# Performance work log

Hardware: AMD Instinct MI355X
Metric: run time of the kernel (lower is better)

The kernel has to match this reference:

```python
import jax, jax.numpy as jnp
import numpy as np

TEMPERATURE = 0.07
NEG_INF = -9e15
EPS = 1e-8  # matches torch F.cosine_similarity eps default


def setup_inputs() -> dict:
    key = jax.random.key(0)
    k1, k2 = jax.random.split(key)
    N, D = 4096, 512
    z1 = jax.random.normal(k1, (N, D), dtype=jnp.float32)
    z2 = jax.random.normal(k2, (N, D), dtype=jnp.float32)
    return {"z1": z1, "z2": z2}


def reference(z1, z2):
    N = z1.shape[0]
    z = jnp.concatenate([z1, z2], axis=0)  # [2N, D]
    # cosine similarity as normalized GEMM (torch clamps norm by eps)
    norm = jnp.maximum(jnp.linalg.norm(z, axis=-1, keepdims=True), EPS)
    zn = z / norm
    sim = (zn @ zn.T) / TEMPERATURE  # [2N, 2N]
    two_n = 2 * N
    idx = jnp.arange(two_n)
    sim = sim.at[idx, idx].set(NEG_INF)
    # positives: diag(sim, N) then diag(sim, -N)
    pos_upper = sim[idx[:N], idx[:N] + N]
    pos_lower = sim[idx[:N] + N, idx[:N]]
    positives = jnp.concatenate([pos_upper, pos_lower], axis=0)  # [2N]
    loss = -positives + jax.scipy.special.logsumexp(sim, axis=1)
    return loss.mean()
```

## Files before the change

kernel.cpp:

```cpp
#include <hip/hip_runtime.h>
#include <hip/hip_bf16.h>

#define N_ROWS 4096
#define TWO_N 8192
#define DIM 512
#define BK 32
#define NKS (DIM / BK)
#define INV_T 14.285714285714286f
#define LOG2E 1.4426950408889634f
#define C_LOG2E 20.60992915555662f
#define INV_SQRT_T 3.7796447300922722f

typedef __bf16 bf16x8 __attribute__((ext_vector_type(8)));
typedef float f32x4 __attribute__((ext_vector_type(4)));

#define ASYNC_COPY16(gp, lp)                                                     \
  __builtin_amdgcn_global_load_lds((const __attribute__((address_space(1))) void*)(gp), \
                                   (__attribute__((address_space(3))) void*)(lp), 16, 0, 0)

#define VMCNT(n) asm volatile("s_waitcnt vmcnt(" #n ")" ::: "memory")

__global__ __launch_bounds__(256) void k_prep(const float* __restrict__ z1,
                                              const float* __restrict__ z2,
                                              __hip_bfloat16* __restrict__ zn,
                                              float* __restrict__ posbuf,
                                              float* __restrict__ rowsum) {
  const int t = threadIdx.x;
  const int wv = t >> 6, lane = t & 63;
  const int r = blockIdx.x * 4 + wv;
  if (blockIdx.x < 32) rowsum[blockIdx.x * 256 + t] = 0.f;

  const float4* p1 = reinterpret_cast<const float4*>(z1 + (size_t)r * DIM) + (lane << 1);
  const float4* p2 = reinterpret_cast<const float4*>(z2 + (size_t)r * DIM) + (lane << 1);
  float4 a0 = p1[0], a1 = p1[1];
  float4 b0 = p2[0], b1 = p2[1];

  float s1 = a0.x * a0.x + a0.y * a0.y + a0.z * a0.z + a0.w * a0.w
           + a1.x * a1.x + a1.y * a1.y + a1.z * a1.z + a1.w * a1.w;
  float s2 = b0.x * b0.x + b0.y * b0.y + b0.z * b0.z + b0.w * b0.w
           + b1.x * b1.x + b1.y * b1.y + b1.z * b1.z + b1.w * b1.w;
  float sd = a0.x * b0.x + a0.y * b0.y + a0.z * b0.z + a0.w * b0.w
           + a1.x * b1.x + a1.y * b1.y + a1.z * b1.z + a1.w * b1.w;
#pragma unroll
  for (int off = 1; off < 64; off <<= 1) {
    s1 += __shfl_xor(s1, off, 64);
    s2 += __shfl_xor(s2, off, 64);
    sd += __shfl_xor(sd, off, 64);
  }
  const float sc1 = INV_SQRT_T / fmaxf(sqrtf(s1), 1e-8f);
  const float sc2 = INV_SQRT_T / fmaxf(sqrtf(s2), 1e-8f);

  bf16x8 o;
  o[0] = (__bf16)(a0.x * sc1); o[1] = (__bf16)(a0.y * sc1);
  o[2] = (__bf16)(a0.z * sc1); o[3] = (__bf16)(a0.w * sc1);
  o[4] = (__bf16)(a1.x * sc1); o[5] = (__bf16)(a1.y * sc1);
  o[6] = (__bf16)(a1.z * sc1); o[7] = (__bf16)(a1.w * sc1);
  *reinterpret_cast<bf16x8*>(zn + (size_t)r * DIM + (lane << 3)) = o;

  o[0] = (__bf16)(b0.x * sc2); o[1] = (__bf16)(b0.y * sc2);
  o[2] = (__bf16)(b0.z * sc2); o[3] = (__bf16)(b0.w * sc2);
  o[4] = (__bf16)(b1.x * sc2); o[5] = (__bf16)(b1.y * sc2);
  o[6] = (__bf16)(b1.z * sc2); o[7] = (__bf16)(b1.w * sc2);
  *reinterpret_cast<bf16x8*>(zn + (size_t)(r + N_ROWS) * DIM + (lane << 3)) = o;

  if (lane == 0) posbuf[r] = sd * sc1 * sc2;
}

__global__ __launch_bounds__(256, 3) void k_lse(const __hip_bfloat16* __restrict__ Zn,
                                                float* __restrict__ rowsum) {
  __shared__ char smem[49152] __attribute__((aligned(16)));
  const int tid  = threadIdx.x;
  const int wave = tid >> 6;
  const int lane = tid & 63;
  const int cl   = lane & 15;
  const int q    = lane >> 4;

  const int b = (blockIdx.x & 7) * 260 + (blockIdx.x >> 3);

  int rt = (int)((129.0f - sqrtf(16641.0f - 8.0f * (float)b)) * 0.5f);
  if (rt > 63) rt = 63;
  if (rt < 0) rt = 0;
  while (rt > 0 && 64 * rt - rt * (rt - 1) / 2 > b) rt--;
  while (64 * (rt + 1) - (rt + 1) * rt / 2 <= b) rt++;
  const int ct = rt + (b - (64 * rt - rt * (rt - 1) / 2));

  const int wr = (wave >> 1) * 64;
  const int wc = (wave & 1) * 64;

  const int g0 = tid, g1 = tid + 256;
  const int r0 = g0 >> 2, k0 = (((g0 & 3) - ((g0 >> 4) & 3)) & 3) * 8;
  const int r1 = g1 >> 2, k1 = (((g1 & 3) - ((g1 >> 4) & 3)) & 3) * 8;
  const size_t aoff0 = (size_t)(rt * 128 + r0) * DIM + k0;
  const size_t aoff1 = (size_t)(rt * 128 + r1) * DIM + k1;
  const size_t boff0 = (size_t)(ct * 128 + r0) * DIM + k0;
  const size_t boff1 = (size_t)(ct * 128 + r1) * DIM + k1;

  f32x4 acc[4][4] = {};
  const int kx = ((q + (cl >> 2)) & 3) * 8;

#define STAGE(bufi, ko)                                                    \
  {                                                                        \
    char* dA = smem + (bufi) * 16384 + wave * 1024;                        \
    char* dB = smem + (bufi) * 16384 + 8192 + wave * 1024;                 \
    ASYNC_COPY16(Zn + aoff0 + (ko), dA);                                   \
    ASYNC_COPY16(Zn + aoff1 + (ko), dA + 4096);                            \
    ASYNC_COPY16(Zn + boff0 + (ko), dB);                                   \
    ASYNC_COPY16(Zn + boff1 + (ko), dB + 4096);                            \
  }

  STAGE(0, 0);
  STAGE(1, BK);
  int cur = 0;
  for (int ks = 0; ks < NKS; ks++) {
    if (ks + 1 < NKS) { VMCNT(4); } else { VMCNT(0); }
    __builtin_amdgcn_s_barrier();
    asm volatile("" ::: "memory");
    if (ks + 2 < NKS) {
      int nb = cur + 2; if (nb >= 3) nb -= 3;
      STAGE(nb, (ks + 2) * BK);
    }

    const char* sA = smem + cur * 16384;
    const char* sB = sA + 8192;
    bf16x8 af[4], bfr[4];
#pragma unroll
    for (int i = 0; i < 4; i++)
      af[i] = *reinterpret_cast<const bf16x8*>(sA + ((wr + i * 16 + cl) * BK + kx) * 2);
#pragma unroll
    for (int j = 0; j < 4; j++)
      bfr[j] = *reinterpret_cast<const bf16x8*>(sB + ((wc + j * 16 + cl) * BK + kx) * 2);
#pragma unroll
    for (int i = 0; i < 4; i++)
#pragma unroll
      for (int j = 0; j < 4; j++)
        acc[i][j] = __builtin_amdgcn_mfma_f32_16x16x32_bf16(af[i], bfr[j], acc[i][j], 0, 0, 0);

    cur = (cur + 1 == 3) ? 0 : cur + 1;
  }
#undef STAGE

  const bool diagw = (rt == ct) && (wr == wc);
  float psum[4][4];
#pragma unroll
  for (int i = 0; i < 4; i++)
#pragma unroll
    for (int r = 0; r < 4; r++) psum[i][r] = 0.f;
  float colp[4] = {0.f, 0.f, 0.f, 0.f};

#pragma unroll
  for (int i = 0; i < 4; i++)
#pragma unroll
    for (int j = 0; j < 4; j++)
#pragma unroll
      for (int r = 0; r < 4; r++) {
        float e = exp2f(fmaf(acc[i][j][r], LOG2E, -C_LOG2E));
        if (diagw && (i == j) && (cl == q * 4 + r)) e = 0.f;
        psum[i][r] += e;
        colp[j] += e;
      }

#pragma unroll
  for (int i = 0; i < 4; i++)
#pragma unroll
    for (int r = 0; r < 4; r++) {
      float v = psum[i][r];
      v += __shfl_xor(v, 1, 64);
      v += __shfl_xor(v, 2, 64);
      v += __shfl_xor(v, 4, 64);
      v += __shfl_xor(v, 8, 64);
      if (cl == 0) atomicAdd(&rowsum[rt * 128 + wr + i * 16 + q * 4 + r], v);
    }

  if (rt != ct) {
#pragma unroll
    for (int j = 0; j < 4; j++) {
      float v = colp[j];
      v += __shfl_xor(v, 16, 64);
      v += __shfl_xor(v, 32, 64);
      if (q == 0) atomicAdd(&rowsum[ct * 128 + wc + j * 16 + cl], v);
    }
  }
}

__global__ void k_final(const float* __restrict__ rowsum, const float* __restrict__ posbuf,
                        float* __restrict__ out) {
  __shared__ float red[16];
  const int t = threadIdx.x;
  float s = 0.f;
#pragma unroll
  for (int it = 0; it < TWO_N / 1024; it++) {
    const int row = it * 1024 + t;
    float v = logf(rowsum[row]);
    if (row < N_ROWS) v -= 2.f * posbuf[row];
    s += v;
  }
#pragma unroll
  for (int off = 32; off > 0; off >>= 1) s += __shfl_down(s, off, 64);
  if ((t & 63) == 0) red[t >> 6] = s;
  __syncthreads();
  if (t == 0) {
    float tot = 0.f;
#pragma unroll
    for (int i = 0; i < 16; i++) tot += red[i];
    out[0] = tot / (float)TWO_N + INV_T;
  }
}

extern "C" void kernel_launch(void* const* d_in, const int* in_sizes, int n_in,
                              void* d_out, int out_size, void* d_ws, size_t ws_size,
                              hipStream_t stream) {
  const float* z1 = (const float*)d_in[0];
  const float* z2 = (const float*)d_in[1];
  float* out = (float*)d_out;
  char* ws = (char*)d_ws;

  __hip_bfloat16* zn = (__hip_bfloat16*)ws;
  float* rowsum = (float*)(ws + 8388608);
  float* posbuf = (float*)(ws + 8421376);

  k_prep<<<1024, 256, 0, stream>>>(z1, z2, zn, posbuf, rowsum);
  k_lse<<<2080, 256, 0, stream>>>(zn, rowsum);
  k_final<<<1, 1024, 0, stream>>>(rowsum, posbuf, out);
}
```

Baseline: 130.3 us.

## Use 256x256 tiles with 8 waves and phased double-buffered LDS pipeline

Moves the symmetric-GEMM LSE kernel from 128x128 tiles with 4 waves to 256x256 tiles with 8 waves, 128 KB of double-buffered LDS, and a BK=64 XOR-swizzled layout. The main loop becomes barrier-separated phases that issue the next stage's async loads alongside the MFMA work, and raise wave priority during the MFMA bursts. The larger tiles are meant to cut global and LDS traffic per flop and the atomic count. In exchange there are only 528 blocks, so fewer tiles to balance across CUs, wasted work on the diagonal tiles, and higher LDS and register use.

```diff
diff --git a/kernel.cpp b/kernel.cpp
--- a/kernel.cpp
+++ b/kernel.cpp
@@ -4,8 +4,6 @@
 #define N_ROWS 4096
 #define TWO_N 8192
 #define DIM 512
-#define BK 32
-#define NKS (DIM / BK)
 #define INV_T 14.285714285714286f
 #define LOG2E 1.4426950408889634f
 #define C_LOG2E 20.60992915555662f
@@ -66,101 +64,122 @@
   if (lane == 0) posbuf[r] = sd * sc1 * sc2;
 }
 
-__global__ __launch_bounds__(256, 3) void k_lse(const __hip_bfloat16* __restrict__ Zn,
+__global__ __launch_bounds__(512, 2) void k_lse(const __hip_bfloat16* __restrict__ Zn,
                                                 float* __restrict__ rowsum) {
-  __shared__ char smem[49152] __attribute__((aligned(16)));
+  __shared__ char smem[131072] __attribute__((aligned(16)));
   const int tid  = threadIdx.x;
   const int wave = tid >> 6;
   const int lane = tid & 63;
   const int cl   = lane & 15;
   const int q    = lane >> 4;
-
-  const int b = (blockIdx.x & 7) * 260 + (blockIdx.x >> 3);
-
-  int rt = (int)((129.0f - sqrtf(16641.0f - 8.0f * (float)b)) * 0.5f);
-  if (rt > 63) rt = 63;
+  const int wm   = wave >> 2;
+  const int wn   = wave & 3;
+
+  const int b = (blockIdx.x & 7) * 66 + (blockIdx.x >> 3);
+  int rt = (int)((65.0f - sqrtf(4225.0f - 8.0f * (float)b)) * 0.5f);
   if (rt < 0) rt = 0;
-  while (rt > 0 && 64 * rt - rt * (rt - 1) / 2 > b) rt--;
-  while (64 * (rt + 1) - (rt + 1) * rt / 2 <= b) rt++;
-  const int ct = rt + (b - (64 * rt - rt * (rt - 1) / 2));
-
-  const int wr = (wave >> 1) * 64;
-  const int wc = (wave & 1) * 64;
-
-  const int g0 = tid, g1 = tid + 256;
-  const int r0 = g0 >> 2, k0 = (((g0 & 3) - ((g0 >> 4) & 3)) & 3) * 8;
-  const int r1 = g1 >> 2, k1 = (((g1 & 3) - ((g1 >> 4) & 3)) & 3) * 8;
-  const size_t aoff0 = (size_t)(rt * 128 + r0) * DIM + k0;
-  const size_t aoff1 = (size_t)(rt * 128 + r1) * DIM + k1;
-  const size_t boff0 = (size_t)(ct * 128 + r0) * DIM + k0;
-  const size_t boff1 = (size_t)(ct * 128 + r1) * DIM + k1;
-
-  f32x4 acc[4][4] = {};
-  const int kx = ((q + (cl >> 2)) & 3) * 8;
-
-#define STAGE(bufi, ko)                                                    \
-  {                                                                        \
-    char* dA = smem + (bufi) * 16384 + wave * 1024;                        \
-    char* dB = smem + (bufi) * 16384 + 8192 + wave * 1024;                 \
-    ASYNC_COPY16(Zn + aoff0 + (ko), dA);                                   \
-    ASYNC_COPY16(Zn + aoff1 + (ko), dA + 4096);                            \
-    ASYNC_COPY16(Zn + boff0 + (ko), dB);                                   \
-    ASYNC_COPY16(Zn + boff1 + (ko), dB + 4096);                            \
-  }
-
-  STAGE(0, 0);
-  STAGE(1, BK);
-  int cur = 0;
-  for (int ks = 0; ks < NKS; ks++) {
-    if (ks + 1 < NKS) { VMCNT(4); } else { VMCNT(0); }
-    __builtin_amdgcn_s_barrier();
-    asm volatile("" ::: "memory");
-    if (ks + 2 < NKS) {
-      int nb = cur + 2; if (nb >= 3) nb -= 3;
-      STAGE(nb, (ks + 2) * BK);
+  if (rt > 31) rt = 31;
+  while (rt > 0 && 32 * rt - rt * (rt - 1) / 2 > b) rt--;
+  while (32 * (rt + 1) - (rt + 1) * rt / 2 <= b) rt++;
+  const int ct = rt + (b - (32 * rt - rt * (rt - 1) / 2));
+
+  const int r0 = tid >> 3;
+  const int gg = (tid & 7) ^ ((tid >> 3) & 7);
+  const __hip_bfloat16* gA = Zn + (size_t)(rt * 256 + r0) * DIM + gg * 8;
+  const __hip_bfloat16* gB = Zn + (size_t)(ct * 256 + r0) * DIM + gg * 8;
+
+  const int xa = ((q ^ (cl & 7)) << 4);
+  const int aBase = (wm * 128 + cl) * 128 + xa;
+  const int bBase = 32768 + (wn * 64 + cl) * 128 + xa;
+
+  f32x4 acc[8][4] = {};
+
+#define STAGE_A(d, kt1)                                                         \
+  ASYNC_COPY16(gA + (kt1) * 64,             smem + (d) * 65536 + wave * 1024);          \
+  ASYNC_COPY16(gA + (kt1) * 64 + 64 * DIM,  smem + (d) * 65536 + wave * 1024 + 8192);   \
+  ASYNC_COPY16(gA + (kt1) * 64 + 128 * DIM, smem + (d) * 65536 + wave * 1024 + 16384);  \
+  ASYNC_COPY16(gA + (kt1) * 64 + 192 * DIM, smem + (d) * 65536 + wave * 1024 + 24576)
+
+#define STAGE_B(d, kt1)                                                         \
+  ASYNC_COPY16(gB + (kt1) * 64,             smem + (d) * 65536 + 32768 + wave * 1024);          \
+  ASYNC_COPY16(gB + (kt1) * 64 + 64 * DIM,  smem + (d) * 65536 + 32768 + wave * 1024 + 8192);   \
+  ASYNC_COPY16(gB + (kt1) * 64 + 128 * DIM, smem + (d) * 65536 + 32768 + wave * 1024 + 16384);  \
+  ASYNC_COPY16(gB + (kt1) * 64 + 192 * DIM, smem + (d) * 65536 + 32768 + wave * 1024 + 24576)
+
+#define PHASE(d, mh, kc, EXTRA1, EXTRA2)                                        \
+  {                                                                             \
+    const char* _sb = smem + (d) * 65536;                                       \
+    bf16x8 af[4], bv[4];                                                        \
+    _Pragma("unroll") for (int i = 0; i < 4; i++)                               \
+      af[i] = *reinterpret_cast<const bf16x8*>(                                 \
+          _sb + ((aBase + (mh) * 8192 + i * 2048) ^ ((kc) * 64)));              \
+    _Pragma("unroll") for (int j = 0; j < 4; j++)                               \
+      bv[j] = *reinterpret_cast<const bf16x8*>(                                 \
+          _sb + ((bBase + j * 2048) ^ ((kc) * 64)));                            \
+    EXTRA1;                                                                     \
+    __builtin_amdgcn_s_barrier();                                               \
+    asm volatile("s_waitcnt lgkmcnt(0)" ::: "memory");                          \
+    __builtin_amdgcn_sched_barrier(0);                                          \
+    __builtin_amdgcn_s_setprio(1);                                              \
+    _Pragma("unroll") for (int i = 0; i < 4; i++)                               \
+      _Pragma("unroll") for (int j = 0; j < 4; j++)                             \
+        acc[(mh) * 4 + i][j] = __builtin_amdgcn_mfma_f32_16x16x32_bf16(         \
+            af[i], bv[j], acc[(mh) * 4 + i][j], 0, 0, 0);                       \
+    __builtin_amdgcn_s_setprio(0);                                              \
+    EXTRA2;                                                                     \
+    __builtin_amdgcn_s_barrier();                                               \
+  }
+
+  STAGE_A(0, 0);
+  STAGE_B(0, 0);
+  VMCNT(0);
+  __builtin_amdgcn_s_barrier();
+
+#pragma unroll
+  for (int it = 0; it < 4; ++it) {
+    const int khi = 2 * it + 1;
+    PHASE(0, 0, 0, STAGE_A(1, khi), );
+    PHASE(0, 0, 1, STAGE_B(1, khi), );
+    PHASE(0, 1, 0, , );
+    PHASE(0, 1, 1, , VMCNT(0));
+    if (it < 3) {
+      PHASE(1, 0, 0, STAGE_A(0, khi + 1), );
+      PHASE(1, 0, 1, STAGE_B(0, khi + 1), );
+      PHASE(1, 1, 0, , );
+      PHASE(1, 1, 1, , VMCNT(0));
+    } else {
+      PHASE(1, 0, 0, , );
+      PHASE(1, 0, 1, , );
+      PHASE(1, 1, 0, , );
+      PHASE(1, 1, 1, , );
     }
-
-    const char* sA = smem + cur * 16384;
-    const char* sB = sA + 8192;
-    bf16x8 af[4], bfr[4];
-#pragma unroll
-    for (int i = 0; i < 4; i++)
-      af[i] = *reinterpret_cast<const bf16x8*>(sA + ((wr + i * 16 + cl) * BK + kx) * 2);
-#pragma unroll
-    for (int j = 0; j < 4; j++)
-      bfr[j] = *reinterpret_cast<const bf16x8*>(sB + ((wc + j * 16 + cl) * BK + kx) * 2);
-#pragma unroll
-    for (int i = 0; i < 4; i++)
-#pragma unroll
-      for (int j = 0; j < 4; j++)
-        acc[i][j] = __builtin_amdgcn_mfma_f32_16x16x32_bf16(af[i], bfr[j], acc[i][j], 0, 0, 0);
-
-    cur = (cur + 1 == 3) ? 0 : cur + 1;
-  }
-#undef STAGE
-
-  const bool diagw = (rt == ct) && (wr == wc);
-  float psum[4][4];
-#pragma unroll
-  for (int i = 0; i < 4; i++)
+  }
+#undef PHASE
+#undef STAGE_A
+#undef STAGE_B
+
+  const bool dt = (rt == ct);
+  float psum[8][4];
+#pragma unroll
+  for (int i = 0; i < 8; i++)
 #pragma unroll
     for (int r = 0; r < 4; r++) psum[i][r] = 0.f;
   float colp[4] = {0.f, 0.f, 0.f, 0.f};
 
 #pragma unroll
-  for (int i = 0; i < 4; i++)
+  for (int i = 0; i < 8; i++)
 #pragma unroll
     for (int j = 0; j < 4; j++)
 #pragma unroll
       for (int r = 0; r < 4; r++) {
         float e = exp2f(fmaf(acc[i][j][r], LOG2E, -C_LOG2E));
-        if (diagw && (i == j) && (cl == q * 4 + r)) e = 0.f;
+        if (dt && (wm * 128 + i * 16 + q * 4 + r) == (wn * 64 + j * 16 + cl)) e = 0.f;
         psum[i][r] += e;
         colp[j] += e;
       }
 
 #pragma unroll
-  for (int i = 0; i < 4; i++)
+  for (int i = 0; i < 8; i++)
 #pragma unroll
     for (int r = 0; r < 4; r++) {
       float v = psum[i][r];
@@ -168,16 +187,16 @@
       v += __shfl_xor(v, 2, 64);
       v += __shfl_xor(v, 4, 64);
       v += __shfl_xor(v, 8, 64);
-      if (cl == 0) atomicAdd(&rowsum[rt * 128 + wr + i * 16 + q * 4 + r], v);
+      if (cl == 0) atomicAdd(&rowsum[rt * 256 + wm * 128 + i * 16 + q * 4 + r], v);
     }
 
-  if (rt != ct) {
+  if (!dt) {
 #pragma unroll
     for (int j = 0; j < 4; j++) {
       float v = colp[j];
       v += __shfl_xor(v, 16, 64);
       v += __shfl_xor(v, 32, 64);
-      if (q == 0) atomicAdd(&rowsum[ct * 128 + wc + j * 16 + cl], v);
+      if (q == 0) atomicAdd(&rowsum[ct * 256 + wn * 64 + j * 16 + cl], v);
     }
   }
 }
@@ -219,6 +238,6 @@
   float* posbuf = (float*)(ws + 8421376);
 
   k_prep<<<1024, 256, 0, stream>>>(z1, z2, zn, posbuf, rowsum);
-  k_lse<<<2080, 256, 0, stream>>>(zn, rowsum);
+  k_lse<<<528, 512, 0, stream>>>(zn, rowsum);
   k_final<<<1, 1024, 0, stream>>>(rowsum, posbuf, out);
 }
```

Measured after the change: 160.5 us. +23.1%, slower.

## Process two column tiles per block to reuse A tile in symmetric LSE GEMM

Applied to the files above, without the earlier changes.

Each block of the upper-triangular similarity GEMM now computes one 128-row tile against two adjacent 128-column tiles. The A tile is loaded once per k-step and shared across both, which halves block count and A-tile traffic. The change also swaps the LDS swizzle to an XOR pattern, fully unrolls the k loop, and raises wave priority around the MFMA burst. In exchange it uses more LDS and registers (occupancy target drops from 3 to 2 blocks per CU), and the last column pair in each row may be half-empty, wasting its MFMAs.

```diff
diff --git a/kernel.cpp b/kernel.cpp
--- a/kernel.cpp
+++ b/kernel.cpp
@@ -66,86 +66,94 @@
   if (lane == 0) posbuf[r] = sd * sc1 * sc2;
 }
 
-__global__ __launch_bounds__(256, 3) void k_lse(const __hip_bfloat16* __restrict__ Zn,
+__global__ __launch_bounds__(256, 2) void k_lse(const __hip_bfloat16* __restrict__ Zn,
                                                 float* __restrict__ rowsum) {
-  __shared__ char smem[49152] __attribute__((aligned(16)));
+  __shared__ char smem[73728] __attribute__((aligned(16)));
   const int tid  = threadIdx.x;
   const int wave = tid >> 6;
   const int lane = tid & 63;
   const int cl   = lane & 15;
   const int q    = lane >> 4;
 
-  const int b = (blockIdx.x & 7) * 260 + (blockIdx.x >> 3);
-
-  int rt = (int)((129.0f - sqrtf(16641.0f - 8.0f * (float)b)) * 0.5f);
+  const int b = (blockIdx.x & 7) * 132 + (blockIdx.x >> 3);
+
+#define CUM(r) (((r) >> 1) * (65 - ((r) >> 1)) + (((r) & 1) ? (32 - ((r) >> 1)) : 0))
+  int rt = 65 - (int)sqrtf(4225.0f - 4.0f * (float)b);
+  if (rt < 0) rt = 0;
   if (rt > 63) rt = 63;
-  if (rt < 0) rt = 0;
-  while (rt > 0 && 64 * rt - rt * (rt - 1) / 2 > b) rt--;
-  while (64 * (rt + 1) - (rt + 1) * rt / 2 <= b) rt++;
-  const int ct = rt + (b - (64 * rt - rt * (rt - 1) / 2));
+  while (rt > 0 && CUM(rt) > b) rt--;
+  while (rt < 63 && CUM(rt + 1) <= b) rt++;
+  const int k = b - CUM(rt);
+#undef CUM
+  const int ctA = rt + 2 * k;
+  const int ctB = ctA + 1;
+  const bool hasB = (ctB < 64);
+  const int ctBs = hasB ? ctB : ctA;
 
   const int wr = (wave >> 1) * 64;
   const int wc = (wave & 1) * 64;
 
-  const int g0 = tid, g1 = tid + 256;
-  const int r0 = g0 >> 2, k0 = (((g0 & 3) - ((g0 >> 4) & 3)) & 3) * 8;
-  const int r1 = g1 >> 2, k1 = (((g1 & 3) - ((g1 >> 4) & 3)) & 3) * 8;
-  const size_t aoff0 = (size_t)(rt * 128 + r0) * DIM + k0;
-  const size_t aoff1 = (size_t)(rt * 128 + r1) * DIM + k1;
-  const size_t boff0 = (size_t)(ct * 128 + r0) * DIM + k0;
-  const size_t boff1 = (size_t)(ct * 128 + r1) * DIM + k1;
-
-  f32x4 acc[4][4] = {};
-  const int kx = ((q + (cl >> 2)) & 3) * 8;
-
-#define STAGE(bufi, ko)                                                    \
-  {                                                                        \
-    char* dA = smem + (bufi) * 16384 + wave * 1024;                        \
-    char* dB = smem + (bufi) * 16384 + 8192 + wave * 1024;                 \
-    ASYNC_COPY16(Zn + aoff0 + (ko), dA);                                   \
-    ASYNC_COPY16(Zn + aoff1 + (ko), dA + 4096);                            \
-    ASYNC_COPY16(Zn + boff0 + (ko), dB);                                   \
-    ASYNC_COPY16(Zn + boff1 + (ko), dB + 4096);                            \
+  const int r0  = tid >> 2;
+  const int kg0 = (tid & 3) ^ ((tid >> 3) & 3);
+  const __hip_bfloat16* gA0  = Zn + (size_t)(rt * 128 + r0) * DIM + kg0 * 8;
+  const __hip_bfloat16* gBA0 = Zn + (size_t)(ctA * 128 + r0) * DIM + kg0 * 8;
+  const __hip_bfloat16* gBB0 = Zn + (size_t)(ctBs * 128 + r0) * DIM + kg0 * 8;
+
+  f32x4 acc[4][8] = {};
+  const int kxl = (q ^ ((cl >> 1) & 3)) << 4;
+
+#define STAGE(d, ks1)                                                       \
+  {                                                                         \
+    char* _b = smem + (d) * 24576 + wave * 1024;                            \
+    const int _ko = (ks1) * BK;                                             \
+    ASYNC_COPY16(gA0 + _ko,             _b);                                \
+    ASYNC_COPY16(gA0 + _ko + 64 * DIM,  _b + 4096);                         \
+    ASYNC_COPY16(gBA0 + _ko,            _b + 8192);                         \
+    ASYNC_COPY16(gBA0 + _ko + 64 * DIM, _b + 12288);                        \
+    ASYNC_COPY16(gBB0 + _ko,            _b + 16384);                        \
+    ASYNC_COPY16(gBB0 + _ko + 64 * DIM, _b + 20480);                        \
   }
 
   STAGE(0, 0);
-  STAGE(1, BK);
-  int cur = 0;
+  STAGE(1, 1);
+#pragma unroll
   for (int ks = 0; ks < NKS; ks++) {
-    if (ks + 1 < NKS) { VMCNT(4); } else { VMCNT(0); }
+    const int cur = ks % 3;
+    if (ks + 1 < NKS) { VMCNT(6); } else { VMCNT(0); }
     __builtin_amdgcn_s_barrier();
     asm volatile("" ::: "memory");
-    if (ks + 2 < NKS) {
-      int nb = cur + 2; if (nb >= 3) nb -= 3;
-      STAGE(nb, (ks + 2) * BK);
-    }
-
-    const char* sA = smem + cur * 16384;
-    const char* sB = sA + 8192;
-    bf16x8 af[4], bfr[4];
+    if (ks + 2 < NKS) STAGE((ks + 2) % 3, ks + 2);
+
+    const char* sA  = smem + cur * 24576;
+    const char* sB0 = sA + 8192;
+    const char* sB1 = sA + 16384;
+    bf16x8 af[4], bfr[8];
 #pragma unroll
     for (int i = 0; i < 4; i++)
-      af[i] = *reinterpret_cast<const bf16x8*>(sA + ((wr + i * 16 + cl) * BK + kx) * 2);
-#pragma unroll
-    for (int j = 0; j < 4; j++)
-      bfr[j] = *reinterpret_cast<const bf16x8*>(sB + ((wc + j * 16 + cl) * BK + kx) * 2);
+      af[i] = *reinterpret_cast<const bf16x8*>(sA + (wr + i * 16 + cl) * 64 + kxl);
+#pragma unroll
+    for (int j = 0; j < 4; j++) {
+      bfr[j]     = *reinterpret_cast<const bf16x8*>(sB0 + (wc + j * 16 + cl) * 64 + kxl);
+      bfr[4 + j] = *reinterpret_cast<const bf16x8*>(sB1 + (wc + j * 16 + cl) * 64 + kxl);
+    }
+    __builtin_amdgcn_s_setprio(1);
 #pragma unroll
     for (int i = 0; i < 4; i++)
 #pragma unroll
-      for (int j = 0; j < 4; j++)
+      for (int j = 0; j < 8; j++)
         acc[i][j] = __builtin_amdgcn_mfma_f32_16x16x32_bf16(af[i], bfr[j], acc[i][j], 0, 0, 0);
-
-    cur = (cur + 1 == 3) ? 0 : cur + 1;
+    __builtin_amdgcn_s_setprio(0);
   }
 #undef STAGE
 
-  const bool diagw = (rt == ct) && (wr == wc);
+  const bool diagw = (rt == ctA) && (wr == wc);
   float psum[4][4];
 #pragma unroll
   for (int i = 0; i < 4; i++)
 #pragma unroll
     for (int r = 0; r < 4; r++) psum[i][r] = 0.f;
-  float colp[4] = {0.f, 0.f, 0.f, 0.f};
+  float colpA[4] = {0.f, 0.f, 0.f, 0.f};
+  float colpB[4] = {0.f, 0.f, 0.f, 0.f};
 
 #pragma unroll
   for (int i = 0; i < 4; i++)
@@ -156,8 +164,20 @@
         float e = exp2f(fmaf(acc[i][j][r], LOG2E, -C_LOG2E));
         if (diagw && (i == j) && (cl == q * 4 + r)) e = 0.f;
         psum[i][r] += e;
-        colp[j] += e;
+        colpA[j] += e;
       }
+  if (hasB) {
+#pragma unroll
+    for (int i = 0; i < 4; i++)
+#pragma unroll
+      for (int j = 0; j < 4; j++)
+#pragma unroll
+        for (int r = 0; r < 4; r++) {
+          float e = exp2f(fmaf(acc[i][4 + j][r], LOG2E, -C_LOG2E));
+          psum[i][r] += e;
+          colpB[j] += e;
+        }
+  }
 
 #pragma unroll
   for (int i = 0; i < 4; i++)
@@ -171,13 +191,22 @@
       if (cl == 0) atomicAdd(&rowsum[rt * 128 + wr + i * 16 + q * 4 + r], v);
     }
 
-  if (rt != ct) {
+  if (rt != ctA) {
 #pragma unroll
     for (int j = 0; j < 4; j++) {
-      float v = colp[j];
+      float v = colpA[j];
       v += __shfl_xor(v, 16, 64);
       v += __shfl_xor(v, 32, 64);
-      if (q == 0) atomicAdd(&rowsum[ct * 128 + wc + j * 16 + cl], v);
+      if (q == 0) atomicAdd(&rowsum[ctA * 128 + wc + j * 16 + cl], v);
+    }
+  }
+  if (hasB) {
+#pragma unroll
+    for (int j = 0; j < 4; j++) {
+      float v = colpB[j];
+      v += __shfl_xor(v, 16, 64);
+      v += __shfl_xor(v, 32, 64);
+      if (q == 0) atomicAdd(&rowsum[ctB * 128 + wc + j * 16 + cl], v);
     }
   }
 }
@@ -219,6 +248,6 @@
   float* posbuf = (float*)(ws + 8421376);
 
   k_prep<<<1024, 256, 0, stream>>>(z1, z2, zn, posbuf, rowsum);
-  k_lse<<<2080, 256, 0, stream>>>(zn, rowsum);
+  k_lse<<<1056, 256, 0, stream>>>(zn, rowsum);
   k_final<<<1, 1024, 0, stream>>>(rowsum, posbuf, out);
 }
```

New measurement: 125.3 us. -3.8%, faster.

## Switch k_lse to double-buffered LDS with XOR swizzle and four blocks per CU

Applied to the files above, without the earlier changes.

The GEMM+exp kernel drops from a three-stage LDS ring to two buffers, cutting shared memory from 48KB to 32KB and raising launch bounds to allow four resident blocks per CU. The LDS layout changes from a rotation-based swizzle to an XOR swizzle, and the k-loop is fully unrolled. Each iteration now prefetches only one stage ahead and waits for it before the barrier, so latency hiding relies more on the extra occupancy than on prefetch depth. The tighter register budget from the higher launch bound could cause spills.

```diff
diff --git a/kernel.cpp b/kernel.cpp
--- a/kernel.cpp
+++ b/kernel.cpp
@@ -66,9 +66,9 @@
   if (lane == 0) posbuf[r] = sd * sc1 * sc2;
 }
 
-__global__ __launch_bounds__(256, 3) void k_lse(const __hip_bfloat16* __restrict__ Zn,
+__global__ __launch_bounds__(256, 4) void k_lse(const __hip_bfloat16* __restrict__ Zn,
                                                 float* __restrict__ rowsum) {
-  __shared__ char smem[49152] __attribute__((aligned(16)));
+  __shared__ char smem[32768] __attribute__((aligned(16)));
   const int tid  = threadIdx.x;
   const int wave = tid >> 6;
   const int lane = tid & 63;
@@ -87,55 +87,50 @@
   const int wr = (wave >> 1) * 64;
   const int wc = (wave & 1) * 64;
 
-  const int g0 = tid, g1 = tid + 256;
-  const int r0 = g0 >> 2, k0 = (((g0 & 3) - ((g0 >> 4) & 3)) & 3) * 8;
-  const int r1 = g1 >> 2, k1 = (((g1 & 3) - ((g1 >> 4) & 3)) & 3) * 8;
-  const size_t aoff0 = (size_t)(rt * 128 + r0) * DIM + k0;
-  const size_t aoff1 = (size_t)(rt * 128 + r1) * DIM + k1;
-  const size_t boff0 = (size_t)(ct * 128 + r0) * DIM + k0;
-  const size_t boff1 = (size_t)(ct * 128 + r1) * DIM + k1;
+  const int r0  = tid >> 2;
+  const int kg0 = (tid & 3) ^ ((tid >> 3) & 3);
+  const __hip_bfloat16* gA0 = Zn + (size_t)(rt * 128 + r0) * DIM + kg0 * 8;
+  const __hip_bfloat16* gB0 = Zn + (size_t)(ct * 128 + r0) * DIM + kg0 * 8;
 
   f32x4 acc[4][4] = {};
-  const int kx = ((q + (cl >> 2)) & 3) * 8;
-
-#define STAGE(bufi, ko)                                                    \
-  {                                                                        \
-    char* dA = smem + (bufi) * 16384 + wave * 1024;                        \
-    char* dB = smem + (bufi) * 16384 + 8192 + wave * 1024;                 \
-    ASYNC_COPY16(Zn + aoff0 + (ko), dA);                                   \
-    ASYNC_COPY16(Zn + aoff1 + (ko), dA + 4096);                            \
-    ASYNC_COPY16(Zn + boff0 + (ko), dB);                                   \
-    ASYNC_COPY16(Zn + boff1 + (ko), dB + 4096);                            \
+  const int kxl = (q ^ ((cl >> 1) & 3)) << 4;
+
+#define STAGE(d, ks1)                                                       \
+  {                                                                         \
+    char* _b = smem + (d) * 16384 + wave * 1024;                            \
+    const int _ko = (ks1) * BK;                                             \
+    ASYNC_COPY16(gA0 + _ko,            _b);                                 \
+    ASYNC_COPY16(gA0 + _ko + 64 * DIM, _b + 4096);                          \
+    ASYNC_COPY16(gB0 + _ko,            _b + 8192);                          \
+    ASYNC_COPY16(gB0 + _ko + 64 * DIM, _b + 12288);                         \
   }
 
   STAGE(0, 0);
-  STAGE(1, BK);
-  int cur = 0;
+  VMCNT(0);
+  __builtin_amdgcn_s_barrier();
+
+#pragma unroll
   for (int ks = 0; ks < NKS; ks++) {
-    if (ks + 1 < NKS) { VMCNT(4); } else { VMCNT(0); }
-    __builtin_amdgcn_s_barrier();
-    asm volatile("" ::: "memory");
-    if (ks + 2 < NKS) {
-      int nb = cur + 2; if (nb >= 3) nb -= 3;
-      STAGE(nb, (ks + 2) * BK);
-    }
+    const int cur = ks & 1;
+    if (ks + 1 < NKS) STAGE(cur ^ 1, ks + 1);
 
     const char* sA = smem + cur * 16384;
     const char* sB = sA + 8192;
     bf16x8 af[4], bfr[4];
 #pragma unroll
     for (int i = 0; i < 4; i++)
-      af[i] = *reinterpret_cast<const bf16x8*>(sA + ((wr + i * 16 + cl) * BK + kx) * 2);
+      af[i] = *reinterpret_cast<const bf16x8*>(sA + (wr + i * 16 + cl) * 64 + kxl);
 #pragma unroll
     for (int j = 0; j < 4; j++)
-      bfr[j] = *reinterpret_cast<const bf16x8*>(sB + ((wc + j * 16 + cl) * BK + kx) * 2);
+      bfr[j] = *reinterpret_cast<const bf16x8*>(sB + (wc + j * 16 + cl) * 64 + kxl);
 #pragma unroll
     for (int i = 0; i < 4; i++)
 #pragma unroll
       for (int j = 0; j < 4; j++)
         acc[i][j] = __builtin_amdgcn_mfma_f32_16x16x32_bf16(af[i], bfr[j], acc[i][j], 0, 0, 0);
 
-    cur = (cur + 1 == 3) ? 0 : cur + 1;
+    if (ks + 1 < NKS) VMCNT(0);
+    __builtin_amdgcn_s_barrier();
   }
 #undef STAGE
 
```

After: 138.5 us. 6.3% more time.
